# Optimization experiments

Measured on AMD Instinct MI355X. Metric: run time of the kernel, lower is better.

The kernel has to match this reference:

```python
import jax, jax.numpy as jnp
import numpy as np

N_NODES = 100000
N_EDGES = 1600000
IN_DIM, FEAT_DIM, HID_DIM, OUT_DIM = 256, 128, 128, 128


def _glorot(key, shape):
    lim = float(np.sqrt(6.0 / (shape[0] + shape[1])))
    return jax.random.uniform(key, shape, jnp.float32, -lim, lim)


def setup_inputs() -> dict:
    key = jax.random.key(0)
    ks = jax.random.split(key, 6)
    x = jax.random.normal(ks[0], (N_NODES, IN_DIM), jnp.float32)
    edge_index = jax.random.randint(ks[1], (2, N_EDGES), 0, N_NODES, dtype=jnp.int64)
    return {
        "x": x,
        "edge_index": edge_index,
        "Wp": _glorot(ks[2], (IN_DIM, FEAT_DIM)),
        "bp": jnp.zeros((FEAT_DIM,), jnp.float32),
        "W1": _glorot(ks[3], (FEAT_DIM, HID_DIM)),
        "b1": jnp.zeros((HID_DIM,), jnp.float32),
        "W2": _glorot(ks[4], (HID_DIM, OUT_DIM)),
        "b2": jnp.zeros((OUT_DIM,), jnp.float32),
    }


def _gcn_conv(h, W, b, src, dst, norm, deg_inv, n):
    # PyG GCNConv: linear first, symmetric-normalized aggregation (with
    # self-loops), bias after aggregation. Self-loop term = z_i / deg_i.
    z = h @ W                                   # [N, out]
    msg = (norm[src] * norm[dst])[:, None] * z[src]  # [E, out]
    agg = jax.ops.segment_sum(msg, dst, num_segments=n)
    return agg + z * deg_inv[:, None] + b


def reference(x, edge_index, Wp, bp, W1, b1, W2, b2):
    src, dst = edge_index[0], edge_index[1]
    n = x.shape[0]
    # degrees on A + I (self-loop adds 1)
    deg = jax.ops.segment_sum(jnp.ones(src.shape[0], x.dtype), dst, num_segments=n) + 1.0
    norm = jax.lax.rsqrt(deg)
    deg_inv = 1.0 / deg
    h = x @ Wp + bp                              # feature_pre linear
    h = jax.nn.relu(_gcn_conv(h, W1, b1, src, dst, norm, deg_inv, n))
    # dropout is identity in eval mode; layer_num=2 -> no hidden convs
    return _gcn_conv(h, W2, b2, src, dst, norm, deg_inv, n)
```

## Files before the change

kernel.cpp:

```cpp
#include <hip/hip_runtime.h>
#include <cstdint>
#include <cstddef>

#define N_NODES 100000
#define N_EDGES 1600000

constexpr int NPB = 512;
constexpr int NBUCK = (N_NODES + NPB - 1) / NPB;
constexpr int EPB = 8192;
constexpr int NCHUNK = (N_EDGES + EPB - 1) / EPB;

typedef _Float16 half8 __attribute__((ext_vector_type(8)));
typedef _Float16 half2v __attribute__((ext_vector_type(2)));
typedef float f32x4 __attribute__((ext_vector_type(4)));

__global__ __launch_bounds__(256) void b1_hist(const int* __restrict__ dst,
                                               int* __restrict__ bbc) {
    __shared__ int hist[NBUCK];
    int t = threadIdx.x;
    if (t < NBUCK) hist[t] = 0;
    __syncthreads();
    int base = blockIdx.x * EPB;
#pragma unroll
    for (int i = 0; i < EPB / 256; ++i) {
        int e = base + i * 256 + t;
        if (e < N_EDGES) atomicAdd(&hist[dst[e] >> 9], 1);
    }
    __syncthreads();
    if (t < NBUCK) bbc[t * NCHUNK + blockIdx.x] = hist[t];
}

__global__ void b_scan(int* __restrict__ bbc, int* __restrict__ bucketOff,
                       int* __restrict__ rowStart) {
    __shared__ int tot[NBUCK];
    int t = threadIdx.x;
    if (t < NBUCK) {
        int run = 0;
        for (int blk = 0; blk < NCHUNK; ++blk) {
            int idx = t * NCHUNK + blk;
            int c = bbc[idx];
            bbc[idx] = run;
            run += c;
        }
        tot[t] = run;
    }
    __syncthreads();
    if (t == 0) {
        int acc = 0;
        for (int b = 0; b < NBUCK; ++b) {
            bucketOff[b] = acc;
            acc += tot[b];
        }
        bucketOff[NBUCK] = acc;
        rowStart[N_NODES] = acc;
    }
}

__global__ __launch_bounds__(256) void b2_scatter(const int* __restrict__ src,
                                                  const int* __restrict__ dst,
                                                  const int* __restrict__ bbc,
                                                  const int* __restrict__ bucketOff,
                                                  int* __restrict__ staged) {
    __shared__ int cnt[NBUCK];
    __shared__ int base[NBUCK];
    int t = threadIdx.x;
    if (t < NBUCK) {
        cnt[t] = 0;
        base[t] = bucketOff[t] + bbc[t * NCHUNK + blockIdx.x];
    }
    __syncthreads();
    int ebase = blockIdx.x * EPB;
#pragma unroll
    for (int i = 0; i < EPB / 256; ++i) {
        int e = ebase + i * 256 + t;
        if (e < N_EDGES) {
            int d = dst[e];
            int b = d >> 9;
            int r = atomicAdd(&cnt[b], 1);
            staged[base[b] + r] = ((d & 511) << 17) | src[e];
        }
    }
}

__global__ __launch_bounds__(256) void b3_sort(const int* __restrict__ staged,
                                               const int* __restrict__ bucketOff,
                                               int* __restrict__ rowStart,
                                               float* __restrict__ normv,
                                               int* __restrict__ colIdx) {
    __shared__ int hist[NPB];
    __shared__ int sc0[NPB], sc1[NPB];
    __shared__ int cursor[NPB];
    int t = threadIdx.x;
    int b = blockIdx.x;
    int e0 = bucketOff[b], e1 = bucketOff[b + 1];
    int ne = e1 - e0;
    int node0 = b * NPB;
    int nn = min(NPB, N_NODES - node0);

    for (int j = t; j < NPB; j += 256) hist[j] = 0;
    __syncthreads();
    for (int idx = t; idx < ne; idx += 256)
        atomicAdd(&hist[staged[e0 + idx] >> 17], 1);
    __syncthreads();
    for (int j = t; j < NPB; j += 256) sc0[j] = hist[j];
    __syncthreads();
    int* s = sc0;
    int* d = sc1;
    for (int off = 1; off < NPB; off <<= 1) {
        for (int j = t; j < NPB; j += 256) d[j] = s[j] + (j >= off ? s[j - off] : 0);
        __syncthreads();
        int* tmp = s; s = d; d = tmp;
    }
    for (int j = t; j < NPB; j += 256) {
        int excl = s[j] - hist[j];
        cursor[j] = excl;
        if (j < nn) {
            rowStart[node0 + j] = e0 + excl;
            normv[node0 + j] = (float)(1.0 / sqrt((double)(hist[j] + 1)));
        }
    }
    __syncthreads();
    for (int idx = t; idx < ne; idx += 256) {
        int v = staged[e0 + idx];
        int dl = v >> 17;
        int sn = v & 0x1FFFF;
        int r = atomicAdd(&cursor[dl], 1);
        colIdx[e0 + r] = sn;
    }
}

__global__ void wc_kernel(const float* __restrict__ Wp, const float* __restrict__ bp,
                          const float* __restrict__ W1, float* __restrict__ Wc,
                          float* __restrict__ bc) {
    int r = blockIdx.x;
    int cc = threadIdx.x;
    float acc = 0.f;
    if (r < 256) {
        for (int k = 0; k < 128; ++k) acc = fmaf(Wp[r * 128 + k], W1[k * 128 + cc], acc);
        Wc[r * 128 + cc] = acc;
    } else {
        for (int k = 0; k < 128; ++k) acc = fmaf(bp[k], W1[k * 128 + cc], acc);
        bc[cc] = acc;
    }
}

__global__ void tsplit_kernel(const float* __restrict__ W, _Float16* __restrict__ Oh,
                              _Float16* __restrict__ Ol, int K) {
    int id = blockIdx.x * 256 + threadIdx.x;
    if (id >= K * 128) return;
    int n = id / K;
    int k = id - n * K;
    float v = W[k * 128 + n];
    _Float16 h = (_Float16)v;
    Oh[id] = h;
    Ol[id] = (_Float16)(v - (float)h);
}

template <bool AF16, int K>
__global__ __launch_bounds__(256, 2) void mfma_gemm(const float* __restrict__ Af,
                                                    const _Float16* __restrict__ Ah,
                                                    const _Float16* __restrict__ Bth,
                                                    const _Float16* __restrict__ Btl,
                                                    const float* __restrict__ bias,
                                                    const float* __restrict__ scale,
                                                    float* __restrict__ Cf,
                                                    _Float16* __restrict__ Ch,
                                                    int M) {
    constexpr int NSLAB = K / 32;
    __shared__ _Float16 sBh[2][128 * 40];
    __shared__ _Float16 sBl[2][128 * 40];

    const int t = threadIdx.x;
    const int w = t >> 6;
    const int wm = w & 1;
    const int wn = w >> 1;
    const int lane = t & 63;
    const int q = lane >> 4;
    const int mr = lane & 15;
    const int row0 = blockIdx.x * 128 + wm * 64;
    const int col0 = wn * 64;

    const int sn = t >> 1;
    const int sseg = t & 1;
    const _Float16* gBh = Bth + (size_t)sn * K + sseg * 16;
    const _Float16* gBl = Btl + (size_t)sn * K + sseg * 16;
    const int swoff = sn * 40 + sseg * 16;

    int arow[4];
#pragma unroll
    for (int mt = 0; mt < 4; ++mt) {
        int r = row0 + mt * 16 + mr;
        arow[mt] = (r < M) ? r : (M - 1);
    }

    f32x4 acc[4][4];
#pragma unroll
    for (int mt = 0; mt < 4; ++mt)
#pragma unroll
        for (int nt = 0; nt < 4; ++nt) acc[mt][nt] = (f32x4){0.f, 0.f, 0.f, 0.f};

    {
        half8 h0 = *(const half8*)(gBh);
        half8 h1 = *(const half8*)(gBh + 8);
        half8 l0 = *(const half8*)(gBl);
        half8 l1 = *(const half8*)(gBl + 8);
        *(half8*)&sBh[0][swoff] = h0;
        *(half8*)&sBh[0][swoff + 8] = h1;
        *(half8*)&sBl[0][swoff] = l0;
        *(half8*)&sBl[0][swoff + 8] = l1;
    }
    float4 aPre0[4], aPre1[4];
    half8  aPreH[4];
#pragma unroll
    for (int mt = 0; mt < 4; ++mt) {
        if constexpr (AF16) {
            aPreH[mt] = *(const half8*)(Ah + (size_t)arow[mt] * K + q * 8);
        } else {
            const float* ap = Af + (size_t)arow[mt] * K + q * 8;
            aPre0[mt] = *(const float4*)ap;
            aPre1[mt] = *(const float4*)(ap + 4);
        }
    }
    __syncthreads();

#pragma unroll
    for (int s = 0; s < NSLAB; ++s) {
        const int cur = s & 1;
        const int nxt = 1 - cur;

        half8 ah[4], al[4];
#pragma unroll
        for (int mt = 0; mt < 4; ++mt) {
            if constexpr (AF16) {
                ah[mt] = aPreH[mt];
            } else {
                float av[8] = {aPre0[mt].x, aPre0[mt].y, aPre0[mt].z, aPre0[mt].w,
                               aPre1[mt].x, aPre1[mt].y, aPre1[mt].z, aPre1[mt].w};
#pragma unroll
                for (int j = 0; j < 8; ++j) {
                    _Float16 h = (_Float16)av[j];
                    ah[mt][j] = h;
                    al[mt][j] = (_Float16)(av[j] - (float)h);
                }
            }
        }

        half8 nh0, nh1, nl0, nl1;
        if (s + 1 < NSLAB) {
            const int ko = (s + 1) * 32;
            nh0 = *(const half8*)(gBh + ko);
            nh1 = *(const half8*)(gBh + ko + 8);
            nl0 = *(const half8*)(gBl + ko);
            nl1 = *(const half8*)(gBl + ko + 8);
#pragma unroll
            for (int mt = 0; mt < 4; ++mt) {
                if constexpr (AF16) {
                    aPreH[mt] = *(const half8*)(Ah + (size_t)arow[mt] * K + ko + q * 8);
                } else {
                    const float* ap = Af + (size_t)arow[mt] * K + ko + q * 8;
                    aPre0[mt] = *(const float4*)ap;
                    aPre1[mt] = *(const float4*)(ap + 4);
                }
            }
        }

        half8 bh[4], bl[4];
#pragma unroll
        for (int nt = 0; nt < 4; ++nt) {
            int n = col0 + nt * 16 + mr;
            bh[nt] = *(half8*)&sBh[cur][n * 40 + q * 8];
            bl[nt] = *(half8*)&sBl[cur][n * 40 + q * 8];
        }

#pragma unroll
        for (int mt = 0; mt < 4; ++mt)
#pragma unroll
            for (int nt = 0; nt < 4; ++nt) {
                acc[mt][nt] = __builtin_amdgcn_mfma_f32_16x16x32_f16(ah[mt], bh[nt], acc[mt][nt], 0, 0, 0);
                acc[mt][nt] = __builtin_amdgcn_mfma_f32_16x16x32_f16(ah[mt], bl[nt], acc[mt][nt], 0, 0, 0);
                if constexpr (!AF16)
                    acc[mt][nt] = __builtin_amdgcn_mfma_f32_16x16x32_f16(al[mt], bh[nt], acc[mt][nt], 0, 0, 0);
            }

        if (s + 1 < NSLAB) {
            *(half8*)&sBh[nxt][swoff] = nh0;
            *(half8*)&sBh[nxt][swoff + 8] = nh1;
            *(half8*)&sBl[nxt][swoff] = nl0;
            *(half8*)&sBl[nxt][swoff + 8] = nl1;
            __syncthreads();
        }
    }

#pragma unroll
    for (int mt = 0; mt < 4; ++mt) {
#pragma unroll
        for (int r = 0; r < 4; ++r) {
            int row = row0 + mt * 16 + q * 4 + r;
            if (row >= M) continue;
            float sc = scale[row];
#pragma unroll
            for (int nt = 0; nt < 4; ++nt) {
                int col = col0 + nt * 16 + mr;
                float bv = bias ? bias[col] : 0.f;
                float val = (acc[mt][nt][r] + bv) * sc;
                if (Ch) Ch[(size_t)row * 128 + col] = (_Float16)val;
                else    Cf[(size_t)row * 128 + col] = val;
            }
        }
    }
}

__global__ __launch_bounds__(256) void agg_kernel(const _Float16* __restrict__ zs,
                                                  const int* __restrict__ rowStart,
                                                  const int* __restrict__ colIdx,
                                                  const float* __restrict__ normv,
                                                  const float* __restrict__ bias,
                                                  float* __restrict__ outF,
                                                  _Float16* __restrict__ outH,
                                                  int doRelu) {
    int wid = (blockIdx.x * 256 + threadIdx.x) >> 6;
    int lane = threadIdx.x & 63;
    if (wid >= N_NODES) return;
    int s0 = rowStart[wid];
    int s1 = rowStart[wid + 1];
    const int c = lane * 2;
    const _Float16* zc = zs + c;

    float2 a0 = make_float2(0.f, 0.f), a1 = a0, a2 = a0, a3 = a0;
    int e = s0;
    for (; e + 8 <= s1; e += 8) {
        int i0 = colIdx[e + 0], i1 = colIdx[e + 1], i2 = colIdx[e + 2], i3 = colIdx[e + 3];
        int i4 = colIdx[e + 4], i5 = colIdx[e + 5], i6 = colIdx[e + 6], i7 = colIdx[e + 7];
        half2v v0 = *(const half2v*)(zc + (size_t)i0 * 128);
        half2v v1 = *(const half2v*)(zc + (size_t)i1 * 128);
        half2v v2 = *(const half2v*)(zc + (size_t)i2 * 128);
        half2v v3 = *(const half2v*)(zc + (size_t)i3 * 128);
        half2v v4 = *(const half2v*)(zc + (size_t)i4 * 128);
        half2v v5 = *(const half2v*)(zc + (size_t)i5 * 128);
        half2v v6 = *(const half2v*)(zc + (size_t)i6 * 128);
        half2v v7 = *(const half2v*)(zc + (size_t)i7 * 128);
        a0.x += (float)v0[0] + (float)v4[0]; a0.y += (float)v0[1] + (float)v4[1];
        a1.x += (float)v1[0] + (float)v5[0]; a1.y += (float)v1[1] + (float)v5[1];
        a2.x += (float)v2[0] + (float)v6[0]; a2.y += (float)v2[1] + (float)v6[1];
        a3.x += (float)v3[0] + (float)v7[0]; a3.y += (float)v3[1] + (float)v7[1];
    }
    if (e + 4 <= s1) {
        int i0 = colIdx[e + 0], i1 = colIdx[e + 1], i2 = colIdx[e + 2], i3 = colIdx[e + 3];
        half2v v0 = *(const half2v*)(zc + (size_t)i0 * 128);
        half2v v1 = *(const half2v*)(zc + (size_t)i1 * 128);
        half2v v2 = *(const half2v*)(zc + (size_t)i2 * 128);
        half2v v3 = *(const half2v*)(zc + (size_t)i3 * 128);
        a0.x += (float)v0[0]; a0.y += (float)v0[1];
        a1.x += (float)v1[0]; a1.y += (float)v1[1];
        a2.x += (float)v2[0]; a2.y += (float)v2[1];
        a3.x += (float)v3[0]; a3.y += (float)v3[1];
        e += 4;
    }
    for (; e < s1; ++e) {
        int i0 = colIdx[e];
        half2v v0 = *(const half2v*)(zc + (size_t)i0 * 128);
        a0.x += (float)v0[0]; a0.y += (float)v0[1];
    }

    half2v self = *(const half2v*)(zc + (size_t)wid * 128);
    float sx = (a0.x + a1.x) + (a2.x + a3.x) + (float)self[0];
    float sy = (a0.y + a1.y) + (a2.y + a3.y) + (float)self[1];
    float nd = normv[wid];
    float2 bv = *(const float2*)(bias + c);
    float ox = fmaf(nd, sx, bv.x);
    float oy = fmaf(nd, sy, bv.y);
    if (doRelu) {
        ox = fmaxf(ox, 0.f);
        oy = fmaxf(oy, 0.f);
    }
    if (outH) {
        half2v o;
        o[0] = (_Float16)ox;
        o[1] = (_Float16)oy;
        *(half2v*)(outH + (size_t)wid * 128 + c) = o;
    } else {
        *(float2*)(outF + (size_t)wid * 128 + c) = make_float2(ox, oy);
    }
}

extern "C" void kernel_launch(void* const* d_in, const int* in_sizes, int n_in,
                              void* d_out, int out_size, void* d_ws, size_t ws_size,
                              hipStream_t stream) {
    const float* x  = (const float*)d_in[0];
    const int* ei   = (const int*)d_in[1];
    const float* Wp = (const float*)d_in[2];
    const float* bp = (const float*)d_in[3];
    const float* W1 = (const float*)d_in[4];
    const float* b1 = (const float*)d_in[5];
    const float* W2 = (const float*)d_in[6];
    const float* b2 = (const float*)d_in[7];
    float* out = (float*)d_out;

    const int* srcIdx = ei;
    const int* dstIdx = ei + N_EDGES;

    size_t off = 0;
    auto alloc = [&](size_t bytes) -> void* {
        void* p = (char*)d_ws + off;
        off += (bytes + 511) & ~(size_t)511;
        return p;
    };
    int* rowStart   = (int*)alloc((size_t)(N_NODES + 1) * 4);
    int* colIdx     = (int*)alloc((size_t)N_EDGES * 4);
    int* staged     = (int*)alloc((size_t)N_EDGES * 4);
    int* bbc        = (int*)alloc((size_t)NBUCK * NCHUNK * 4);
    int* bucketOff  = (int*)alloc((size_t)(NBUCK + 1) * 4);
    float* normv    = (float*)alloc((size_t)N_NODES * 4);
    float* Wc       = (float*)alloc((size_t)256 * 128 * 4);
    float* bc       = (float*)alloc((size_t)128 * 4);
    _Float16* Wcth  = (_Float16*)alloc((size_t)128 * 256 * 2);
    _Float16* Wctl  = (_Float16*)alloc((size_t)128 * 256 * 2);
    _Float16* W2th  = (_Float16*)alloc((size_t)128 * 128 * 2);
    _Float16* W2tl  = (_Float16*)alloc((size_t)128 * 128 * 2);
    _Float16* zA    = (_Float16*)alloc((size_t)N_NODES * 128 * 2);
    _Float16* zB    = (_Float16*)alloc((size_t)N_NODES * 128 * 2);

    const int GB = (N_NODES + 127) / 128;
    const int AB = (N_NODES + 3) / 4;

    b1_hist<<<NCHUNK, 256, 0, stream>>>(dstIdx, bbc);
    b_scan<<<1, 256, 0, stream>>>(bbc, bucketOff, rowStart);
    b2_scatter<<<NCHUNK, 256, 0, stream>>>(srcIdx, dstIdx, bbc, bucketOff, staged);
    b3_sort<<<NBUCK, 256, 0, stream>>>(staged, bucketOff, rowStart, normv, colIdx);

    wc_kernel<<<257, 128, 0, stream>>>(Wp, bp, W1, Wc, bc);
    tsplit_kernel<<<(256 * 128 + 255) / 256, 256, 0, stream>>>(Wc, Wcth, Wctl, 256);
    tsplit_kernel<<<(128 * 128 + 255) / 256, 256, 0, stream>>>(W2, W2th, W2tl, 128);

    mfma_gemm<false, 256><<<GB, 256, 0, stream>>>(x, nullptr, Wcth, Wctl, bc, normv,
                                                  nullptr, zA, N_NODES);
    agg_kernel<<<AB, 256, 0, stream>>>(zA, rowStart, colIdx, normv, b1, nullptr, zB, 1);
    mfma_gemm<true, 128><<<GB, 256, 0, stream>>>(nullptr, zB, W2th, W2tl, nullptr, normv,
                                                 nullptr, zA, N_NODES);
    agg_kernel<<<AB, 256, 0, stream>>>(zA, rowStart, colIdx, normv, b2, out, nullptr, 0);
}
```

Baseline: 474.2 us.

## Make MFMA GEMM persistent with whole B matrix resident in swizzled LDS

The tiled GEMM is replaced by a persistent kernel with 256 blocks of 512 threads. Each block loads the full transposed hi/lo fp16 weight matrix once into LDS with an XOR swizzle, then loops over 48-row strips per wave. This removes the per-slab B reloads and __syncthreads, and A is double-buffered two slabs ahead in registers. The cost is 128 KB of LDS for K=256, which limits occupancy to one block per CU, plus a larger accumulator set per wave that adds register pressure.

```diff
diff --git a/kernel.cpp b/kernel.cpp
--- a/kernel.cpp
+++ b/kernel.cpp
@@ -157,154 +157,125 @@
 }
 
 template <bool AF16, int K>
-__global__ __launch_bounds__(256, 2) void mfma_gemm(const float* __restrict__ Af,
-                                                    const _Float16* __restrict__ Ah,
-                                                    const _Float16* __restrict__ Bth,
-                                                    const _Float16* __restrict__ Btl,
-                                                    const float* __restrict__ bias,
-                                                    const float* __restrict__ scale,
-                                                    float* __restrict__ Cf,
-                                                    _Float16* __restrict__ Ch,
-                                                    int M) {
+__global__ __launch_bounds__(512, 2) void mfma_gemm_p(
+    const float* __restrict__ Af, const _Float16* __restrict__ Ah,
+    const _Float16* __restrict__ Bth, const _Float16* __restrict__ Btl,
+    const float* __restrict__ bias, const float* __restrict__ scale,
+    _Float16* __restrict__ Ch, int M, int nstrip) {
     constexpr int NSLAB = K / 32;
-    __shared__ _Float16 sBh[2][128 * 40];
-    __shared__ _Float16 sBl[2][128 * 40];
+    constexpr int JROW = K / 8;
+    __shared__ _Float16 sBh[128 * K];
+    __shared__ _Float16 sBl[128 * K];
 
     const int t = threadIdx.x;
-    const int w = t >> 6;
-    const int wm = w & 1;
-    const int wn = w >> 1;
+    for (int idx = t; idx < 128 * JROW; idx += 512) {
+        int n = idx / JROW;
+        int j = idx - n * JROW;
+        int d = n * K + (((j & 7) ^ (n & 7)) << 3) + ((j >> 3) << 6);
+        *(half8*)&sBh[d] = *(const half8*)(Bth + n * K + (j << 3));
+        *(half8*)&sBl[d] = *(const half8*)(Btl + n * K + (j << 3));
+    }
+    __syncthreads();
+
     const int lane = t & 63;
     const int q = lane >> 4;
     const int mr = lane & 15;
-    const int row0 = blockIdx.x * 128 + wm * 64;
-    const int col0 = wn * 64;
-
-    const int sn = t >> 1;
-    const int sseg = t & 1;
-    const _Float16* gBh = Bth + (size_t)sn * K + sseg * 16;
-    const _Float16* gBl = Btl + (size_t)sn * K + sseg * 16;
-    const int swoff = sn * 40 + sseg * 16;
-
-    int arow[4];
-#pragma unroll
-    for (int mt = 0; mt < 4; ++mt) {
-        int r = row0 + mt * 16 + mr;
-        arow[mt] = (r < M) ? r : (M - 1);
-    }
-
-    f32x4 acc[4][4];
-#pragma unroll
-    for (int mt = 0; mt < 4; ++mt)
-#pragma unroll
-        for (int nt = 0; nt < 4; ++nt) acc[mt][nt] = (f32x4){0.f, 0.f, 0.f, 0.f};
-
-    {
-        half8 h0 = *(const half8*)(gBh);
-        half8 h1 = *(const half8*)(gBh + 8);
-        half8 l0 = *(const half8*)(gBl);
-        half8 l1 = *(const half8*)(gBl + 8);
-        *(half8*)&sBh[0][swoff] = h0;
-        *(half8*)&sBh[0][swoff + 8] = h1;
-        *(half8*)&sBl[0][swoff] = l0;
-        *(half8*)&sBl[0][swoff + 8] = l1;
-    }
-    float4 aPre0[4], aPre1[4];
-    half8  aPreH[4];
-#pragma unroll
-    for (int mt = 0; mt < 4; ++mt) {
-        if constexpr (AF16) {
-            aPreH[mt] = *(const half8*)(Ah + (size_t)arow[mt] * K + q * 8);
-        } else {
-            const float* ap = Af + (size_t)arow[mt] * K + q * 8;
-            aPre0[mt] = *(const float4*)ap;
-            aPre1[mt] = *(const float4*)(ap + 4);
-        }
-    }
-    __syncthreads();
-
-#pragma unroll
-    for (int s = 0; s < NSLAB; ++s) {
-        const int cur = s & 1;
-        const int nxt = 1 - cur;
-
-        half8 ah[4], al[4];
-#pragma unroll
-        for (int mt = 0; mt < 4; ++mt) {
-            if constexpr (AF16) {
-                ah[mt] = aPreH[mt];
-            } else {
-                float av[8] = {aPre0[mt].x, aPre0[mt].y, aPre0[mt].z, aPre0[mt].w,
-                               aPre1[mt].x, aPre1[mt].y, aPre1[mt].z, aPre1[mt].w};
-#pragma unroll
-                for (int j = 0; j < 8; ++j) {
-                    _Float16 h = (_Float16)av[j];
-                    ah[mt][j] = h;
-                    al[mt][j] = (_Float16)(av[j] - (float)h);
+    const int mre = mr & 7;
+    const int gw = (blockIdx.x << 3) + (t >> 6);
+    const int wstride = gridDim.x << 3;
+
+    float bcol[8];
+#pragma unroll
+    for (int nt = 0; nt < 8; ++nt) bcol[nt] = bias ? bias[nt * 16 + mr] : 0.f;
+
+    for (int strip = gw; strip < nstrip; strip += wstride) {
+        const int row0 = strip * 48;
+        int arow[3];
+#pragma unroll
+        for (int mt = 0; mt < 3; ++mt) {
+            int r = row0 + mt * 16 + mr;
+            arow[mt] = (r < M) ? r : (M - 1);
+        }
+
+        f32x4 acc[3][8];
+#pragma unroll
+        for (int mt = 0; mt < 3; ++mt)
+#pragma unroll
+            for (int nt = 0; nt < 8; ++nt) acc[mt][nt] = (f32x4){0.f, 0.f, 0.f, 0.f};
+
+        f32x4 pf[2][3][2];
+        half8 ph[2][3];
+
+#define LOAD_SLAB(SLOT, SS)                                                        \
+        {                                                                          \
+            _Pragma("unroll")                                                      \
+            for (int mt = 0; mt < 3; ++mt) {                                       \
+                if constexpr (AF16) {                                              \
+                    ph[SLOT][mt] =                                                 \
+                        *(const half8*)(Ah + (size_t)arow[mt] * K + (SS) * 32 + q * 8); \
+                } else {                                                           \
+                    const float* ap = Af + (size_t)arow[mt] * K + (SS) * 32 + q * 8; \
+                    pf[SLOT][mt][0] = *(const f32x4*)ap;                           \
+                    pf[SLOT][mt][1] = *(const f32x4*)(ap + 4);                     \
+                }                                                                  \
+            }                                                                      \
+        }
+
+        LOAD_SLAB(0, 0)
+        LOAD_SLAB(1, 1)
+
+#pragma unroll
+        for (int s = 0; s < NSLAB; ++s) {
+            const int sl = s & 1;
+            half8 ah[3], al[3];
+#pragma unroll
+            for (int mt = 0; mt < 3; ++mt) {
+                if constexpr (AF16) {
+                    ah[mt] = ph[sl][mt];
+                } else {
+                    f32x4 a0 = pf[sl][mt][0];
+                    f32x4 a1 = pf[sl][mt][1];
+#pragma unroll
+                    for (int jj = 0; jj < 4; ++jj) {
+                        _Float16 h0 = (_Float16)a0[jj];
+                        _Float16 h1 = (_Float16)a1[jj];
+                        ah[mt][jj] = h0;
+                        ah[mt][jj + 4] = h1;
+                        al[mt][jj] = (_Float16)(a0[jj] - (float)h0);
+                        al[mt][jj + 4] = (_Float16)(a1[jj] - (float)h1);
+                    }
                 }
             }
-        }
-
-        half8 nh0, nh1, nl0, nl1;
-        if (s + 1 < NSLAB) {
-            const int ko = (s + 1) * 32;
-            nh0 = *(const half8*)(gBh + ko);
-            nh1 = *(const half8*)(gBh + ko + 8);
-            nl0 = *(const half8*)(gBl + ko);
-            nl1 = *(const half8*)(gBl + ko + 8);
-#pragma unroll
-            for (int mt = 0; mt < 4; ++mt) {
-                if constexpr (AF16) {
-                    aPreH[mt] = *(const half8*)(Ah + (size_t)arow[mt] * K + ko + q * 8);
-                } else {
-                    const float* ap = Af + (size_t)arow[mt] * K + ko + q * 8;
-                    aPre0[mt] = *(const float4*)ap;
-                    aPre1[mt] = *(const float4*)(ap + 4);
+            if (s + 2 < NSLAB) LOAD_SLAB(sl, s + 2)
+
+            const int kof = ((s >> 1) << 6) + ((((s & 1) << 2) | q) ^ mre) * 8;
+#pragma unroll
+            for (int nt = 0; nt < 8; ++nt) {
+                const int bo = (nt * 16 + mr) * K + kof;
+                half8 bh = *(const half8*)&sBh[bo];
+                half8 bl = *(const half8*)&sBl[bo];
+#pragma unroll
+                for (int mt = 0; mt < 3; ++mt) {
+                    acc[mt][nt] = __builtin_amdgcn_mfma_f32_16x16x32_f16(ah[mt], bh, acc[mt][nt], 0, 0, 0);
+                    acc[mt][nt] = __builtin_amdgcn_mfma_f32_16x16x32_f16(ah[mt], bl, acc[mt][nt], 0, 0, 0);
+                    if constexpr (!AF16)
+                        acc[mt][nt] = __builtin_amdgcn_mfma_f32_16x16x32_f16(al[mt], bh, acc[mt][nt], 0, 0, 0);
                 }
             }
         }
-
-        half8 bh[4], bl[4];
-#pragma unroll
-        for (int nt = 0; nt < 4; ++nt) {
-            int n = col0 + nt * 16 + mr;
-            bh[nt] = *(half8*)&sBh[cur][n * 40 + q * 8];
-            bl[nt] = *(half8*)&sBl[cur][n * 40 + q * 8];
-        }
-
-#pragma unroll
-        for (int mt = 0; mt < 4; ++mt)
-#pragma unroll
-            for (int nt = 0; nt < 4; ++nt) {
-                acc[mt][nt] = __builtin_amdgcn_mfma_f32_16x16x32_f16(ah[mt], bh[nt], acc[mt][nt], 0, 0, 0);
-                acc[mt][nt] = __builtin_amdgcn_mfma_f32_16x16x32_f16(ah[mt], bl[nt], acc[mt][nt], 0, 0, 0);
-                if constexpr (!AF16)
-                    acc[mt][nt] = __builtin_amdgcn_mfma_f32_16x16x32_f16(al[mt], bh[nt], acc[mt][nt], 0, 0, 0);
-            }
-
-        if (s + 1 < NSLAB) {
-            *(half8*)&sBh[nxt][swoff] = nh0;
-            *(half8*)&sBh[nxt][swoff + 8] = nh1;
-            *(half8*)&sBl[nxt][swoff] = nl0;
-            *(half8*)&sBl[nxt][swoff + 8] = nl1;
-            __syncthreads();
-        }
-    }
-
-#pragma unroll
-    for (int mt = 0; mt < 4; ++mt) {
-#pragma unroll
-        for (int r = 0; r < 4; ++r) {
-            int row = row0 + mt * 16 + q * 4 + r;
-            if (row >= M) continue;
-            float sc = scale[row];
-#pragma unroll
-            for (int nt = 0; nt < 4; ++nt) {
-                int col = col0 + nt * 16 + mr;
-                float bv = bias ? bias[col] : 0.f;
-                float val = (acc[mt][nt][r] + bv) * sc;
-                if (Ch) Ch[(size_t)row * 128 + col] = (_Float16)val;
-                else    Cf[(size_t)row * 128 + col] = val;
+#undef LOAD_SLAB
+
+#pragma unroll
+        for (int mt = 0; mt < 3; ++mt) {
+#pragma unroll
+            for (int rr = 0; rr < 4; ++rr) {
+                int row = row0 + mt * 16 + q * 4 + rr;
+                if (row >= M) continue;
+                float sc = scale[row];
+#pragma unroll
+                for (int nt = 0; nt < 8; ++nt)
+                    Ch[(size_t)row * 128 + nt * 16 + mr] =
+                        (_Float16)((acc[mt][nt][rr] + bcol[nt]) * sc);
             }
         }
     }
@@ -420,8 +391,8 @@
     _Float16* zA    = (_Float16*)alloc((size_t)N_NODES * 128 * 2);
     _Float16* zB    = (_Float16*)alloc((size_t)N_NODES * 128 * 2);
 
-    const int GB = (N_NODES + 127) / 128;
     const int AB = (N_NODES + 3) / 4;
+    constexpr int NSTRIP = (N_NODES + 47) / 48;
 
     b1_hist<<<NCHUNK, 256, 0, stream>>>(dstIdx, bbc);
     b_scan<<<1, 256, 0, stream>>>(bbc, bucketOff, rowStart);
@@ -432,10 +403,10 @@
     tsplit_kernel<<<(256 * 128 + 255) / 256, 256, 0, stream>>>(Wc, Wcth, Wctl, 256);
     tsplit_kernel<<<(128 * 128 + 255) / 256, 256, 0, stream>>>(W2, W2th, W2tl, 128);
 
-    mfma_gemm<false, 256><<<GB, 256, 0, stream>>>(x, nullptr, Wcth, Wctl, bc, normv,
-                                                  nullptr, zA, N_NODES);
+    mfma_gemm_p<false, 256><<<256, 512, 0, stream>>>(x, nullptr, Wcth, Wctl, bc, normv,
+                                                     zA, N_NODES, NSTRIP);
     agg_kernel<<<AB, 256, 0, stream>>>(zA, rowStart, colIdx, normv, b1, nullptr, zB, 1);
-    mfma_gemm<true, 128><<<GB, 256, 0, stream>>>(nullptr, zB, W2th, W2tl, nullptr, normv,
-                                                 nullptr, zA, N_NODES);
+    mfma_gemm_p<true, 128><<<256, 512, 0, stream>>>(nullptr, zB, W2th, W2tl, nullptr, normv,
+                                                    zA, N_NODES, NSTRIP);
     agg_kernel<<<AB, 256, 0, stream>>>(zA, rowStart, colIdx, normv, b2, out, nullptr, 0);
 }
```

Result: slower. 637.0 us (+34.3%).
